# Optimization experiments

Measured on AMD Instinct MI355X. Metric: run time of the kernel, lower is better.

Reference implementation:

```python
import jax, jax.numpy as jnp
import numpy as np

DELTA = 1.0

def _lin(x, W, b):
    return x @ W + b

def _node(x, child_c, child_h, Wioux, bioux, Wiouh, biouh, Wfx, bfx, Wfh, bfh):
    # Child-sum TreeLSTM cell. x: [B, D]; child_c, child_h: [B, nc, M]
    h_sum = child_h.sum(axis=1)  # [B, M]
    iou = _lin(x, Wioux, bioux) + _lin(h_sum, Wiouh, biouh)  # [B, 3M]
    i, o, u = jnp.split(iou, 3, axis=-1)
    i, o, u = jax.nn.sigmoid(i), jax.nn.sigmoid(o), jnp.tanh(u)
    # forget gate per child: fh(child_h) + fx(x) broadcast over children
    f = jax.nn.sigmoid(_lin(child_h, Wfh, bfh) + _lin(x, Wfx, bfx)[:, None, :])  # [B, nc, M]
    c = i * u + (f * child_c).sum(axis=1)
    h = o * jnp.tanh(c)
    return c, h

def _treelstm(xs, Wioux, bioux, Wiouh, biouh, Wfx, bfx, Wfh, bfh):
    # xs: [B, 4, D]. Fixed 4-node tree: root = node 3, leaf children = {0,1,2}.
    # All leaves (same depth) are batched into one fused gate GEMM.
    B, _, D = xs.shape
    M = Wfx.shape[1]
    gates = (Wioux, bioux, Wiouh, biouh, Wfx, bfx, Wfh, bfh)
    x_leaf = xs[:, :3].reshape(B * 3, D)
    z = jnp.zeros((B * 3, 1, M), xs.dtype)  # leaves get zero child state
    c_l, h_l = _node(x_leaf, z, z, *gates)
    c_root, h_root = _node(xs[:, 3], c_l.reshape(B, 3, M), h_l.reshape(B, 3, M), *gates)
    return c_root, h_root

def setup_inputs() -> dict:
    key = jax.random.key(0)
    B, L, Lq, V, D, M, H, O = 512, 64, 128, 50000, 512, 512, 256, 30
    ks = jax.random.split(key, 24)
    ri = lambda k, shape: jax.random.randint(k, shape, 0, V)
    rn = lambda k, shape, s: jax.random.normal(k, shape, jnp.float32) * s
    return {
        'q_v': ri(ks[0], (B, L)), 'q_a0': ri(ks[1], (B, L)), 'n_a0': ri(ks[2], (B, L)),
        'q_a1': ri(ks[3], (B, L)), 'n_a1': ri(ks[4], (B, L)), 'q_a2': ri(ks[5], (B, L)),
        'n_a2': ri(ks[6], (B, L)),
        'query': ri(ks[7], (B, Lq)), 'pos': ri(ks[8], (B, Lq)), 'neg': ri(ks[9], (B, Lq)),
        'emb': rn(ks[10], (V, D), 0.02),
        'Wioux': rn(ks[11], (D, 3 * M), D ** -0.5), 'bioux': jnp.zeros((3 * M,), jnp.float32),
        'Wiouh': rn(ks[12], (M, 3 * M), M ** -0.5), 'biouh': jnp.zeros((3 * M,), jnp.float32),
        'Wfx': rn(ks[13], (D, M), D ** -0.5), 'bfx': jnp.zeros((M,), jnp.float32),
        'Wfh': rn(ks[14], (M, M), M ** -0.5), 'bfh': jnp.zeros((M,), jnp.float32),
        'Wwh': rn(ks[15], (M, H), M ** -0.5), 'bwh': jnp.zeros((H,), jnp.float32),
        'Wwp': rn(ks[16], (H, O), H ** -0.5), 'bwp': jnp.zeros((O,), jnp.float32),
    }

def reference(q_v, q_a0, n_a0, q_a1, n_a1, q_a2, n_a2, query, pos, neg,
              emb, Wioux, bioux, Wiouh, biouh, Wfx, bfx, Wfh, bfh, Wwh, bwh, Wwp, bwp):
    D = emb.shape[1]
    pool = lambda ids: emb[ids].mean(axis=1)  # embedding lookup + mean over tokens -> [B, D]
    qv = pool(q_v)
    def trip(qa, na):  # attribute-level triplet hinge loss, per batch row
        return jax.nn.relu(DELTA - (qv * pool(qa)).sum(-1) + (qv * pool(na)).sum(-1))
    loss = trip(q_a0, n_a0) + trip(q_a1, n_a1) + trip(q_a2, n_a2)
    def seq(ids):  # [B, Lq] -> 4 mean-pooled node vectors [B, 4, D]
        e = emb[ids]
        return e.reshape(e.shape[0], 4, -1, D).mean(axis=2)
    gates = (Wioux, bioux, Wiouh, biouh, Wfx, bfx, Wfh, bfh)
    qc, _ = _treelstm(seq(query), *gates)
    pc, _ = _treelstm(seq(pos), *gates)
    nc, _ = _treelstm(seq(neg), *gates)
    sim = lambda l, r: _lin(jax.nn.sigmoid(_lin(l * r, Wwh, bwh)), Wwp, bwp)  # Similarity module
    a = sim(qc, pc).sum(-1)
    b = sim(qc, nc).sum(-1)
    return loss + jax.nn.relu(DELTA - a + b)
```

## Files before the change

### kernel.cpp

```cpp
#include <hip/hip_runtime.h>
#include <hip/hip_bf16.h>


typedef __attribute__((ext_vector_type(8))) short short8;
typedef __attribute__((ext_vector_type(4))) float floatx4;
typedef __attribute__((ext_vector_type(2))) float floatx2;

__device__ inline ushort f2bf(float f) {
    unsigned u = __float_as_uint(f);
    u += 0x7fffu + ((u >> 16) & 1u);
    return (ushort)(u >> 16);
}
__device__ inline float bf2f(ushort u) { return __uint_as_float((unsigned)u << 16); }
__device__ inline float sigm(float x) { return 1.0f / (1.0f + expf(-x)); }

#if defined(__has_builtin)
#if __has_builtin(__builtin_amdgcn_cvt_pk_f32_fp8) && __has_builtin(__builtin_amdgcn_cvt_pk_fp8_f32)
#define HW_FP8 1
#endif
#endif

#ifndef HW_FP8
__device__ inline unsigned enc1(float x) {
    float a = fabsf(x);
    unsigned s = (__float_as_uint(x) >> 31) << 7;
    unsigned b = __float_as_uint(a);
    unsigned uexp = b >> 23;
    if (uexp < 121) {
        int m = (int)(a * 512.0f + 0.5f);
        if (m >= 8) return s | 0x08u;
        return s | (unsigned)m;
    }
    b += 0x00080000u;
    unsigned e = b >> 23;
    if (e > 135u) return s | 0x7Eu;
    return s | ((e - 120u) << 3) | ((b >> 20) & 7u);
}
__device__ inline float dec1(unsigned v) {
    unsigned s = (v >> 7) & 1u, e = (v >> 3) & 15u, m = v & 7u;
    float r = e ? __uint_as_float(((e + 120u) << 23) | (m << 20))
                : (float)m * 0.001953125f;
    return s ? -r : r;
}
#endif

__device__ inline unsigned pk4(float a, float b, float c, float d) {
#ifdef HW_FP8
    int v = 0;
    v = __builtin_amdgcn_cvt_pk_fp8_f32(a, b, v, false);
    v = __builtin_amdgcn_cvt_pk_fp8_f32(c, d, v, true);
    return (unsigned)v;
#else
    return enc1(a) | (enc1(b) << 8) | (enc1(c) << 16) | (enc1(d) << 24);
#endif
}
__device__ inline void dec4_add(unsigned v, float* acc) {
#ifdef HW_FP8
    floatx2 p0 = __builtin_amdgcn_cvt_pk_f32_fp8(v, false);
    floatx2 p1 = __builtin_amdgcn_cvt_pk_f32_fp8(v, true);
    acc[0] += p0[0]; acc[1] += p0[1]; acc[2] += p1[0]; acc[3] += p1[1];
#else
    acc[0] += dec1(v & 255u); acc[1] += dec1((v >> 8) & 255u);
    acc[2] += dec1((v >> 16) & 255u); acc[3] += dec1(v >> 24);
#endif
}

#define GLD16(gp, sp)                                                        \
    __builtin_amdgcn_global_load_lds(                                        \
        (const __attribute__((address_space(1))) unsigned int*)(const void*)(gp), \
        (__attribute__((address_space(3))) unsigned int*)(void*)(sp), 16, 0, 0)

#define FP8_SCALE 64.0f

__global__ __launch_bounds__(256) void prep_all_kernel(
    const float* __restrict__ emb, unsigned char* __restrict__ emb8,
    const float* __restrict__ Wioux, const float* __restrict__ Wiouh,
    const float* __restrict__ Wfh, const float* __restrict__ Wfx,
    const float* __restrict__ Wwh, const float* __restrict__ Wwp,
    const float* __restrict__ bwp,
    ushort* __restrict__ Wcat_t, ushort* __restrict__ Wfh_t,
    ushort* __restrict__ Wfx_t, ushort* __restrict__ Wwh_t,
    float* __restrict__ wsum) {
    __shared__ float tt[32][33];
    int blk = blockIdx.x, tid = threadIdx.x;
    if (blk < 12500) {
        size_t i = ((size_t)blk * 256 + tid) * 8;
        float4 a = *(const float4*)(emb + i);
        float4 b = *(const float4*)(emb + i + 4);
        uint2 o;
        o.x = pk4(a.x * FP8_SCALE, a.y * FP8_SCALE, a.z * FP8_SCALE, a.w * FP8_SCALE);
        o.y = pk4(b.x * FP8_SCALE, b.y * FP8_SCALE, b.z * FP8_SCALE, b.w * FP8_SCALE);
        *(uint2*)(emb8 + i) = o;
        return;
    }
    int tx = tid & 31, ty = tid >> 5;
    if (blk < 14036) {
        int idx = blk - 12500;
        int k0 = (idx & 31) * 32, n0 = (idx >> 5) * 32;
#pragma unroll
        for (int r = 0; r < 4; ++r) {
            int k = k0 + ty + r * 8;
            const float* s = (k < 512) ? Wioux + (size_t)k * 1536
                                       : Wiouh + (size_t)(k - 512) * 1536;
            tt[ty + r * 8][tx] = s[n0 + tx];
        }
        __syncthreads();
#pragma unroll
        for (int r = 0; r < 4; ++r)
            Wcat_t[(size_t)(n0 + ty + r * 8) * 1024 + k0 + tx] = f2bf(tt[tx][ty + r * 8]);
        return;
    }
    if (blk < 14676) {
        const float* W; ushort* Wt; int idx, ncols;
        if (blk < 14292)      { idx = blk - 14036; W = Wfh; Wt = Wfh_t; ncols = 512; }
        else if (blk < 14548) { idx = blk - 14292; W = Wfx; Wt = Wfx_t; ncols = 512; }
        else                  { idx = blk - 14548; W = Wwh; Wt = Wwh_t; ncols = 256; }
        int nt_count = ncols >> 5;
        int k0 = (idx / nt_count) * 32, n0 = (idx % nt_count) * 32;
#pragma unroll
        for (int r = 0; r < 4; ++r)
            tt[ty + r * 8][tx] = W[(size_t)(k0 + ty + r * 8) * ncols + n0 + tx];
        __syncthreads();
#pragma unroll
        for (int r = 0; r < 4; ++r)
            Wt[(size_t)(n0 + ty + r * 8) * 512 + k0 + tx] = f2bf(tt[tx][ty + r * 8]);
        return;
    }
    {
        float s = 0.f;
        for (int o = 0; o < 30; ++o) s += Wwp[tid * 30 + o];
        wsum[tid] = s;
        if (tid == 0) {
            float t = 0.f;
            for (int o = 0; o < 30; ++o) t += bwp[o];
            wsum[256] = t;
        }
    }
}

__global__ __launch_bounds__(256) void mega_gather_kernel(
    const int* __restrict__ q_v,
    const int* __restrict__ qa0, const int* __restrict__ na0,
    const int* __restrict__ qa1, const int* __restrict__ na1,
    const int* __restrict__ qa2, const int* __restrict__ na2,
    const int* __restrict__ query, const int* __restrict__ pos, const int* __restrict__ neg,
    const unsigned char* __restrict__ emb8,
    float* __restrict__ pools, ushort* __restrict__ Xleaf, ushort* __restrict__ XR) {
    __shared__ float sm[256][9];
    int tid = threadIdx.x;
    int c = tid & 63, g = tid >> 6;
    float acc[8] = {};
    if (blockIdx.x < 3584) {
        int s = blockIdx.x >> 9, b = blockIdx.x & 511;
        const int* aptr[7] = {q_v, qa0, na0, qa1, na1, qa2, na2};
        const int* ids = aptr[s] + b * 64 + g * 16;
#pragma unroll 8
        for (int t = 0; t < 16; ++t) {
            const uint2 v = *(const uint2*)(emb8 + (size_t)ids[t] * 512 + c * 8);
            dec4_add(v.x, acc);
            dec4_add(v.y, acc + 4);
        }
#pragma unroll
        for (int k = 0; k < 8; ++k) sm[tid][k] = acc[k];
        __syncthreads();
        if (tid < 64) {
#pragma unroll
            for (int gg = 1; gg < 4; ++gg)
#pragma unroll
                for (int k = 0; k < 8; ++k) acc[k] += sm[tid + gg * 64][k];
            const float sc = 1.0f / (64.0f * FP8_SCALE);
            float* dst = pools + ((size_t)s * 512 + b) * 512 + tid * 8;
            *(float4*)dst = make_float4(acc[0] * sc, acc[1] * sc, acc[2] * sc, acc[3] * sc);
            *(float4*)(dst + 4) = make_float4(acc[4] * sc, acc[5] * sc, acc[6] * sc, acc[7] * sc);
        }
    } else {
        int idx = blockIdx.x - 3584;
        int t = idx >> 11, rem = idx & 2047, b = rem >> 2, node = rem & 3;
        const int* sptr[3] = {query, pos, neg};
        const int* ids = sptr[t] + b * 128 + node * 32 + g * 8;
#pragma unroll
        for (int k = 0; k < 8; ++k) {
            const uint2 v = *(const uint2*)(emb8 + (size_t)ids[k] * 512 + c * 8);
            dec4_add(v.x, acc);
            dec4_add(v.y, acc + 4);
        }
#pragma unroll
        for (int k = 0; k < 8; ++k) sm[tid][k] = acc[k];
        __syncthreads();
        if (tid < 64) {
#pragma unroll
            for (int gg = 1; gg < 4; ++gg)
#pragma unroll
                for (int k = 0; k < 8; ++k) acc[k] += sm[tid + gg * 64][k];
            const float sc = 1.0f / (32.0f * FP8_SCALE);
            short8 o;
#pragma unroll
            for (int k = 0; k < 8; ++k) o[k] = (short)f2bf(acc[k] * sc);
            if (node < 3) {
                size_t r = ((size_t)(t * 512 + b)) * 3 + node;
                *(short8*)(Xleaf + r * 512 + tid * 8) = o;
            } else {
                size_t r = (size_t)(t * 512 + b);
                *(short8*)(XR + r * 1024 + tid * 8) = o;
            }
        }
    }
}

__global__ __launch_bounds__(256) void dots_kernel(const float* __restrict__ pools,
                                                   float* __restrict__ loss) {
    int b = blockIdx.x, tid = threadIdx.x;
    const float* pq = pools + (size_t)b * 512;
    float q0 = pq[tid], q1 = pq[tid + 256];
    float d[6];
#pragma unroll
    for (int a = 0; a < 6; ++a) {
        const float* pa = pools + ((size_t)(a + 1) * 512 + b) * 512;
        d[a] = q0 * pa[tid] + q1 * pa[tid + 256];
    }
    __shared__ float red[6][4];
    int lane = tid & 63, wid = tid >> 6;
#pragma unroll
    for (int a = 0; a < 6; ++a) {
        float v = d[a];
        for (int off = 32; off; off >>= 1) v += __shfl_down(v, off);
        if (lane == 0) red[a][wid] = v;
    }
    __syncthreads();
    if (tid == 0) {
        float l = 0.f;
#pragma unroll
        for (int i = 0; i < 3; ++i) {
            float dq = red[2*i][0] + red[2*i][1] + red[2*i][2] + red[2*i][3];
            float dn = red[2*i+1][0] + red[2*i+1][1] + red[2*i+1][2] + red[2*i+1][3];
            l += fmaxf(0.f, 1.f - dq + dn);
        }
        loss[b] = l;
    }
}

__device__ __forceinline__ void gemm_body(const ushort* __restrict__ A, int lda,
                                          const ushort* __restrict__ Bt, int ldb,
                                          float* __restrict__ C, int ldc, int K,
                                          int bx, int by, ushort* sA, ushort* sB) {
    int tid = threadIdx.x;
    int m0 = bx * 128, n0 = by * 128;
    int w = tid >> 6, lane = tid & 63;
    int wm = (w >> 1) * 64, wn = (w & 1) * 64;
    int l15 = lane & 15, g = lane >> 4;
    int srow = tid >> 2, scol = (tid & 3) * 8;

    const ushort* Ag0 = A + (size_t)(m0 + srow) * lda + scol;
    const ushort* Ag1 = A + (size_t)(m0 + srow + 64) * lda + scol;
    const ushort* Bg0 = Bt + (size_t)(n0 + srow) * ldb + scol;
    const ushort* Bg1 = Bt + (size_t)(n0 + srow + 64) * ldb + scol;
    ushort* sA0 = sA + w * 512;
    ushort* sA1 = sA + 2048 + w * 512;
    ushort* sB0 = sB + w * 512;
    ushort* sB1 = sB + 2048 + w * 512;

    floatx4 acc[4][4] = {};

    for (int kb = 0; kb < K; kb += 32) {
        __syncthreads();
        GLD16(Ag0 + kb, sA0);
        GLD16(Ag1 + kb, sA1);
        GLD16(Bg0 + kb, sB0);
        GLD16(Bg1 + kb, sB1);
        __syncthreads();
        short8 af[4], bf[4];
#pragma unroll
        for (int f = 0; f < 4; ++f) {
            af[f] = *(const short8*)(sA + (wm + f * 16 + l15) * 32 + g * 8);
            bf[f] = *(const short8*)(sB + (wn + f * 16 + l15) * 32 + g * 8);
        }
#pragma unroll
        for (int i = 0; i < 4; ++i)
#pragma unroll
            for (int j = 0; j < 4; ++j)
                acc[i][j] = __builtin_amdgcn_mfma_f32_16x16x32_bf16(af[i], bf[j], acc[i][j], 0, 0, 0);
    }
#pragma unroll
    for (int i = 0; i < 4; ++i)
#pragma unroll
        for (int j = 0; j < 4; ++j) {
            int row = m0 + wm + i * 16 + g * 4;
            int col = n0 + wn + j * 16 + l15;
#pragma unroll
            for (int r = 0; r < 4; ++r)
                C[(size_t)(row + r) * ldc + col] = acc[i][j][r];
        }
}

__global__ __launch_bounds__(256) void gemm_bf16(const ushort* __restrict__ A, int lda,
                                                 const ushort* __restrict__ Bt, int ldb,
                                                 float* __restrict__ C, int ldc, int K) {
    __shared__ alignas(16) ushort sA[128 * 32];
    __shared__ alignas(16) ushort sB[128 * 32];
    gemm_body(A, lda, Bt, ldb, C, ldc, K, blockIdx.x, blockIdx.y, sA, sB);
}

__global__ __launch_bounds__(256) void gemm3_bf16(
    const ushort* __restrict__ h_l, const ushort* __restrict__ XR,
    const ushort* __restrict__ Wfh_t, const ushort* __restrict__ Wfx_t,
    const ushort* __restrict__ Wcat_t,
    float* __restrict__ FH, float* __restrict__ FX, float* __restrict__ IOU_r) {
    __shared__ alignas(16) ushort sA[128 * 32];
    __shared__ alignas(16) ushort sB[128 * 32];
    int r = blockIdx.x;
    if (r < 144)      gemm_body(h_l, 512, Wfh_t, 512, FH, 512, 512, r % 36, r / 36, sA, sB);
    else if (r < 192) { int q = r - 144; gemm_body(XR, 1024, Wfx_t, 512, FX, 512, 512, q % 12, q / 12, sA, sB); }
    else              { int q = r - 192; gemm_body(XR, 1024, Wcat_t, 1024, IOU_r, 1536, 1024, q % 12, q / 12, sA, sB); }
}


__global__ __launch_bounds__(256) void leaf_act_kernel(
    const float* __restrict__ IOU_l, const float* __restrict__ bioux,
    const float* __restrict__ biouh, float* __restrict__ c_l,
    ushort* __restrict__ h_l, ushort* __restrict__ XR) {
    int tb = blockIdx.x, tid = threadIdx.x;
#pragma unroll
    for (int half = 0; half < 2; ++half) {
        int m = tid + half * 256;
        float bi = bioux[m] + biouh[m];
        float bo = bioux[m + 512] + biouh[m + 512];
        float bu = bioux[m + 1024] + biouh[m + 1024];
        float hs = 0.f;
#pragma unroll
        for (int leaf = 0; leaf < 3; ++leaf) {
            size_t r = (size_t)tb * 3 + leaf;
            const float* row = IOU_l + r * 1536;
            float iv = sigm(row[m] + bi);
            float ov = sigm(row[m + 512] + bo);
            float uv = tanhf(row[m + 1024] + bu);
            float c = iv * uv;
            c_l[r * 512 + m] = c;
            float h = ov * tanhf(c);
            h_l[r * 512 + m] = f2bf(h);
            hs += h;
        }
        XR[(size_t)tb * 1024 + 512 + m] = f2bf(hs);
    }
}

__global__ __launch_bounds__(256) void root_act_kernel(
    const float* __restrict__ IOU_r, const float* __restrict__ FH,
    const float* __restrict__ FX, const float* __restrict__ c_l,
    const float* __restrict__ bioux, const float* __restrict__ biouh,
    const float* __restrict__ bfx, const float* __restrict__ bfh,
    float* __restrict__ c_root) {
    int r = blockIdx.x, tid = threadIdx.x;
#pragma unroll
    for (int half = 0; half < 2; ++half) {
        int m = tid + half * 256;
        float iv = sigm(IOU_r[(size_t)r * 1536 + m] + bioux[m] + biouh[m]);
        float uv = tanhf(IOU_r[(size_t)r * 1536 + 1024 + m] + bioux[1024 + m] + biouh[1024 + m]);
        float fx = FX[(size_t)r * 512 + m] + bfx[m];
        float c = iv * uv;
#pragma unroll
        for (int k = 0; k < 3; ++k) {
            size_t idx = ((size_t)r * 3 + k) * 512 + m;
            float f = sigm(FH[idx] + bfh[m] + fx);
            c += f * c_l[idx];
        }
        c_root[(size_t)r * 512 + m] = c;
    }
}

__global__ __launch_bounds__(256) void prod_kernel(const float* __restrict__ c_root,
                                                   ushort* __restrict__ P) {
    int e = blockIdx.x * 256 + threadIdx.x;
    int row = e >> 9, n = e & 511;
    int b = row & 511, which = row >> 9;
    float q = c_root[(size_t)b * 512 + n];
    float o = c_root[((size_t)(which + 1) * 512 + b) * 512 + n];
    P[e] = f2bf(q * o);
}

__global__ __launch_bounds__(256) void final_kernel(
    const float* __restrict__ S, const float* __restrict__ bwh,
    const float* __restrict__ wsum, const float* __restrict__ loss,
    float* __restrict__ out) {
    int b = blockIdx.x, tid = threadIdx.x;
    float w = wsum[tid];
    float bw = bwh[tid];
    float va = sigm(S[(size_t)b * 256 + tid] + bw) * w;
    float vb = sigm(S[(size_t)(512 + b) * 256 + tid] + bw) * w;
    int lane = tid & 63, wid = tid >> 6;
    for (int off = 32; off; off >>= 1) {
        va += __shfl_down(va, off);
        vb += __shfl_down(vb, off);
    }
    __shared__ float ra[4], rb[4];
    if (lane == 0) { ra[wid] = va; rb[wid] = vb; }
    __syncthreads();
    if (tid == 0) {
        float a  = ra[0] + ra[1] + ra[2] + ra[3] + wsum[256];
        float bb = rb[0] + rb[1] + rb[2] + rb[3] + wsum[256];
        out[b] = loss[b] + fmaxf(0.f, 1.f - a + bb);
    }
}


extern "C" void kernel_launch(void* const* d_in, const int* in_sizes, int n_in,
                              void* d_out, int out_size, void* d_ws, size_t ws_size,
                              hipStream_t stream) {
    const int* q_v   = (const int*)d_in[0];
    const int* q_a0  = (const int*)d_in[1];
    const int* n_a0  = (const int*)d_in[2];
    const int* q_a1  = (const int*)d_in[3];
    const int* n_a1  = (const int*)d_in[4];
    const int* q_a2  = (const int*)d_in[5];
    const int* n_a2  = (const int*)d_in[6];
    const int* query = (const int*)d_in[7];
    const int* pos   = (const int*)d_in[8];
    const int* neg   = (const int*)d_in[9];
    const float* emb   = (const float*)d_in[10];
    const float* Wioux = (const float*)d_in[11];
    const float* bioux = (const float*)d_in[12];
    const float* Wiouh = (const float*)d_in[13];
    const float* biouh = (const float*)d_in[14];
    const float* Wfx   = (const float*)d_in[15];
    const float* bfx   = (const float*)d_in[16];
    const float* Wfh   = (const float*)d_in[17];
    const float* bfh   = (const float*)d_in[18];
    const float* Wwh   = (const float*)d_in[19];
    const float* bwh   = (const float*)d_in[20];
    const float* Wwp   = (const float*)d_in[21];
    const float* bwp   = (const float*)d_in[22];
    float* out = (float*)d_out;

    char* w = (char*)d_ws;
    size_t off = 0;
    auto alloc = [&](size_t bytes) -> void* {
        void* p = (void*)(w + off);
        off = (off + bytes + 255) & ~(size_t)255;
        return p;
    };
    ushort* Wcat_t = (ushort*)alloc((size_t)1536 * 1024 * 2);
    ushort* Wfh_t  = (ushort*)alloc((size_t)512 * 512 * 2);
    ushort* Wfx_t  = (ushort*)alloc((size_t)512 * 512 * 2);
    ushort* Wwh_t  = (ushort*)alloc((size_t)256 * 512 * 2);
    float*  wsum   = (float*) alloc(257 * 4);
    float*  lossv  = (float*) alloc(512 * 4);
    ushort* Xleaf  = (ushort*)alloc((size_t)4608 * 512 * 2);
    ushort* XR     = (ushort*)alloc((size_t)1536 * 1024 * 2);
    size_t xbase = off;
    unsigned char* emb8 = (unsigned char*)alloc((size_t)50000 * 512);
    float* pools        = (float*)        alloc((size_t)7 * 512 * 512 * 4);
    off = xbase;
    float*  IOU_l  = (float*) alloc((size_t)4608 * 1536 * 4);
    float*  c_l    = (float*) alloc((size_t)4608 * 512 * 4);
    ushort* h_l    = (ushort*)alloc((size_t)4608 * 512 * 2);
    float*  FH     = (float*) alloc((size_t)4608 * 512 * 4);
    float*  FX     = (float*) alloc((size_t)1536 * 512 * 4);
    float*  IOU_r  = (float*) alloc((size_t)1536 * 1536 * 4);
    float*  c_root = (float*) alloc((size_t)1536 * 512 * 4);
    ushort* P      = (ushort*)alloc((size_t)1024 * 512 * 2);
    float*  S      = (float*) alloc((size_t)1024 * 256 * 4);

    prep_all_kernel<<<14677, 256, 0, stream>>>(emb, emb8, Wioux, Wiouh, Wfh, Wfx, Wwh,
                                               Wwp, bwp, Wcat_t, Wfh_t, Wfx_t, Wwh_t, wsum);
    mega_gather_kernel<<<9728, 256, 0, stream>>>(q_v, q_a0, n_a0, q_a1, n_a1, q_a2, n_a2,
                                                 query, pos, neg, emb8, pools, Xleaf, XR);
    dots_kernel<<<512, 256, 0, stream>>>(pools, lossv);

    gemm_bf16<<<dim3(36, 12), 256, 0, stream>>>(Xleaf, 512, Wcat_t, 1024, IOU_l, 1536, 512);
    leaf_act_kernel<<<1536, 256, 0, stream>>>(IOU_l, bioux, biouh, c_l, h_l, XR);
    gemm3_bf16<<<336, 256, 0, stream>>>(h_l, XR, Wfh_t, Wfx_t, Wcat_t, FH, FX, IOU_r);
    root_act_kernel<<<1536, 256, 0, stream>>>(IOU_r, FH, FX, c_l, bioux, biouh, bfx, bfh, c_root);

    prod_kernel<<<2048, 256, 0, stream>>>(c_root, P);
    gemm_bf16<<<dim3(8, 2), 256, 0, stream>>>(P, 512, Wwh_t, 512, S, 256, 512);
    final_kernel<<<512, 256, 0, stream>>>(S, bwh, wsum, lossv, out);
}
```

Measured before the change: 134.3 us.

## Double-buffer GEMMs, store intermediates in bf16, fuse dots and prod into GEMMs

Gather loops now issue all embedding loads before decoding, to get more memory-level parallelism. The GEMM body double-buffers its LDS tiles so the next K-slice loads while MFMAs run on the current one. The dots reduction is merged into the leaf GEMM launch, and the elementwise product is computed inside the similarity GEMM's A staging, which removes two launches. IOU, FH, FX and c_l intermediates are stored as bf16 to halve their traffic, at some cost in precision.

```diff
diff --git a/kernel.cpp b/kernel.cpp
--- a/kernel.cpp
+++ b/kernel.cpp
@@ -154,12 +154,12 @@
         int s = blockIdx.x >> 9, b = blockIdx.x & 511;
         const int* aptr[7] = {q_v, qa0, na0, qa1, na1, qa2, na2};
         const int* ids = aptr[s] + b * 64 + g * 16;
-#pragma unroll 8
-        for (int t = 0; t < 16; ++t) {
-            const uint2 v = *(const uint2*)(emb8 + (size_t)ids[t] * 512 + c * 8);
-            dec4_add(v.x, acc);
-            dec4_add(v.y, acc + 4);
-        }
+        uint2 v[16];
+#pragma unroll
+        for (int t = 0; t < 16; ++t)
+            v[t] = *(const uint2*)(emb8 + (size_t)ids[t] * 512 + c * 8);
+#pragma unroll
+        for (int t = 0; t < 16; ++t) { dec4_add(v[t].x, acc); dec4_add(v[t].y, acc + 4); }
 #pragma unroll
         for (int k = 0; k < 8; ++k) sm[tid][k] = acc[k];
         __syncthreads();
@@ -178,12 +178,12 @@
         int t = idx >> 11, rem = idx & 2047, b = rem >> 2, node = rem & 3;
         const int* sptr[3] = {query, pos, neg};
         const int* ids = sptr[t] + b * 128 + node * 32 + g * 8;
-#pragma unroll
-        for (int k = 0; k < 8; ++k) {
-            const uint2 v = *(const uint2*)(emb8 + (size_t)ids[k] * 512 + c * 8);
-            dec4_add(v.x, acc);
-            dec4_add(v.y, acc + 4);
-        }
+        uint2 v[8];
+#pragma unroll
+        for (int k = 0; k < 8; ++k)
+            v[k] = *(const uint2*)(emb8 + (size_t)ids[k] * 512 + c * 8);
+#pragma unroll
+        for (int k = 0; k < 8; ++k) { dec4_add(v[k].x, acc); dec4_add(v[k].y, acc + 4); }
 #pragma unroll
         for (int k = 0; k < 8; ++k) sm[tid][k] = acc[k];
         __syncthreads();
@@ -207,41 +207,13 @@
     }
 }
 
-__global__ __launch_bounds__(256) void dots_kernel(const float* __restrict__ pools,
-                                                   float* __restrict__ loss) {
-    int b = blockIdx.x, tid = threadIdx.x;
-    const float* pq = pools + (size_t)b * 512;
-    float q0 = pq[tid], q1 = pq[tid + 256];
-    float d[6];
-#pragma unroll
-    for (int a = 0; a < 6; ++a) {
-        const float* pa = pools + ((size_t)(a + 1) * 512 + b) * 512;
-        d[a] = q0 * pa[tid] + q1 * pa[tid + 256];
-    }
-    __shared__ float red[6][4];
-    int lane = tid & 63, wid = tid >> 6;
-#pragma unroll
-    for (int a = 0; a < 6; ++a) {
-        float v = d[a];
-        for (int off = 32; off; off >>= 1) v += __shfl_down(v, off);
-        if (lane == 0) red[a][wid] = v;
-    }
-    __syncthreads();
-    if (tid == 0) {
-        float l = 0.f;
-#pragma unroll
-        for (int i = 0; i < 3; ++i) {
-            float dq = red[2*i][0] + red[2*i][1] + red[2*i][2] + red[2*i][3];
-            float dn = red[2*i+1][0] + red[2*i+1][1] + red[2*i+1][2] + red[2*i+1][3];
-            l += fmaxf(0.f, 1.f - dq + dn);
-        }
-        loss[b] = l;
-    }
-}
-
+__device__ inline void cstore(float* C, size_t idx, float v)  { C[idx] = v; }
+__device__ inline void cstore(ushort* C, size_t idx, float v) { C[idx] = f2bf(v); }
+
+template <typename OutT>
 __device__ __forceinline__ void gemm_body(const ushort* __restrict__ A, int lda,
                                           const ushort* __restrict__ Bt, int ldb,
-                                          float* __restrict__ C, int ldc, int K,
+                                          OutT* __restrict__ C, int ldc, int K,
                                           int bx, int by, ushort* sA, ushort* sB) {
     int tid = threadIdx.x;
     int m0 = bx * 128, n0 = by * 128;
@@ -254,31 +226,38 @@
     const ushort* Ag1 = A + (size_t)(m0 + srow + 64) * lda + scol;
     const ushort* Bg0 = Bt + (size_t)(n0 + srow) * ldb + scol;
     const ushort* Bg1 = Bt + (size_t)(n0 + srow + 64) * ldb + scol;
-    ushort* sA0 = sA + w * 512;
-    ushort* sA1 = sA + 2048 + w * 512;
-    ushort* sB0 = sB + w * 512;
-    ushort* sB1 = sB + 2048 + w * 512;
 
     floatx4 acc[4][4] = {};
 
+    auto stage = [&](int buf, int kb) {
+        ushort* dA = sA + buf * 4096;
+        ushort* dB = sB + buf * 4096;
+        GLD16(Ag0 + kb, dA + w * 512);
+        GLD16(Ag1 + kb, dA + 2048 + w * 512);
+        GLD16(Bg0 + kb, dB + w * 512);
+        GLD16(Bg1 + kb, dB + 2048 + w * 512);
+    };
+
+    stage(0, 0);
+    __syncthreads();
+    int cur = 0;
     for (int kb = 0; kb < K; kb += 32) {
-        __syncthreads();
-        GLD16(Ag0 + kb, sA0);
-        GLD16(Ag1 + kb, sA1);
-        GLD16(Bg0 + kb, sB0);
-        GLD16(Bg1 + kb, sB1);
-        __syncthreads();
+        if (kb + 32 < K) stage(cur ^ 1, kb + 32);
+        const ushort* bA = sA + cur * 4096;
+        const ushort* bB = sB + cur * 4096;
         short8 af[4], bf[4];
 #pragma unroll
         for (int f = 0; f < 4; ++f) {
-            af[f] = *(const short8*)(sA + (wm + f * 16 + l15) * 32 + g * 8);
-            bf[f] = *(const short8*)(sB + (wn + f * 16 + l15) * 32 + g * 8);
+            af[f] = *(const short8*)(bA + (wm + f * 16 + l15) * 32 + g * 8);
+            bf[f] = *(const short8*)(bB + (wn + f * 16 + l15) * 32 + g * 8);
         }
 #pragma unroll
         for (int i = 0; i < 4; ++i)
 #pragma unroll
             for (int j = 0; j < 4; ++j)
                 acc[i][j] = __builtin_amdgcn_mfma_f32_16x16x32_bf16(af[i], bf[j], acc[i][j], 0, 0, 0);
+        __syncthreads();
+        cur ^= 1;
     }
 #pragma unroll
     for (int i = 0; i < 4; ++i)
@@ -288,35 +267,141 @@
             int col = n0 + wn + j * 16 + l15;
 #pragma unroll
             for (int r = 0; r < 4; ++r)
-                C[(size_t)(row + r) * ldc + col] = acc[i][j][r];
-        }
-}
-
-__global__ __launch_bounds__(256) void gemm_bf16(const ushort* __restrict__ A, int lda,
-                                                 const ushort* __restrict__ Bt, int ldb,
-                                                 float* __restrict__ C, int ldc, int K) {
-    __shared__ alignas(16) ushort sA[128 * 32];
-    __shared__ alignas(16) ushort sB[128 * 32];
-    gemm_body(A, lda, Bt, ldb, C, ldc, K, blockIdx.x, blockIdx.y, sA, sB);
-}
-
-__global__ __launch_bounds__(256) void gemm3_bf16(
+                cstore(C, (size_t)(row + r) * ldc + col, acc[i][j][r]);
+        }
+}
+
+__global__ __launch_bounds__(256) void g1_dots_kernel(
+    const ushort* __restrict__ Xleaf, const ushort* __restrict__ Wcat_t,
+    ushort* __restrict__ IOU_l,
+    const float* __restrict__ pools, float* __restrict__ lossv) {
+    __shared__ alignas(16) ushort sA[8192];
+    __shared__ alignas(16) ushort sB[8192];
+    __shared__ float red[6][4];
+    int blk = blockIdx.x, tid = threadIdx.x;
+    if (blk < 432) {
+        gemm_body(Xleaf, 512, Wcat_t, 1024, IOU_l, 1536, 512, blk % 36, blk / 36, sA, sB);
+        return;
+    }
+    int b = blk - 432;
+    const float* pq = pools + (size_t)b * 512;
+    float q0 = pq[tid], q1 = pq[tid + 256];
+    float d[6];
+#pragma unroll
+    for (int a = 0; a < 6; ++a) {
+        const float* pa = pools + ((size_t)(a + 1) * 512 + b) * 512;
+        d[a] = q0 * pa[tid] + q1 * pa[tid + 256];
+    }
+    int lane = tid & 63, wid = tid >> 6;
+#pragma unroll
+    for (int a = 0; a < 6; ++a) {
+        float v = d[a];
+        for (int off = 32; off; off >>= 1) v += __shfl_down(v, off);
+        if (lane == 0) red[a][wid] = v;
+    }
+    __syncthreads();
+    if (tid == 0) {
+        float l = 0.f;
+#pragma unroll
+        for (int i = 0; i < 3; ++i) {
+            float dq = red[2*i][0] + red[2*i][1] + red[2*i][2] + red[2*i][3];
+            float dn = red[2*i+1][0] + red[2*i+1][1] + red[2*i+1][2] + red[2*i+1][3];
+            l += fmaxf(0.f, 1.f - dq + dn);
+        }
+        lossv[b] = l;
+    }
+}
+
+__global__ __launch_bounds__(256) void gemm3_kernel(
     const ushort* __restrict__ h_l, const ushort* __restrict__ XR,
     const ushort* __restrict__ Wfh_t, const ushort* __restrict__ Wfx_t,
     const ushort* __restrict__ Wcat_t,
-    float* __restrict__ FH, float* __restrict__ FX, float* __restrict__ IOU_r) {
-    __shared__ alignas(16) ushort sA[128 * 32];
-    __shared__ alignas(16) ushort sB[128 * 32];
+    ushort* __restrict__ FH, ushort* __restrict__ FX, ushort* __restrict__ IOU_r) {
+    __shared__ alignas(16) ushort sA[8192];
+    __shared__ alignas(16) ushort sB[8192];
     int r = blockIdx.x;
-    if (r < 144)      gemm_body(h_l, 512, Wfh_t, 512, FH, 512, 512, r % 36, r / 36, sA, sB);
-    else if (r < 192) { int q = r - 144; gemm_body(XR, 1024, Wfx_t, 512, FX, 512, 512, q % 12, q / 12, sA, sB); }
-    else              { int q = r - 192; gemm_body(XR, 1024, Wcat_t, 1024, IOU_r, 1536, 1024, q % 12, q / 12, sA, sB); }
+    if (r < 144)      gemm_body(XR, 1024, Wcat_t, 1024, IOU_r, 1536, 1024, r % 12, r / 12, sA, sB);
+    else if (r < 288) { int q = r - 144; gemm_body(h_l, 512, Wfh_t, 512, FH, 512, 512, q % 36, q / 36, sA, sB); }
+    else              { int q = r - 288; gemm_body(XR, 1024, Wfx_t, 512, FX, 512, 512, q % 12, q / 12, sA, sB); }
+}
+
+__global__ __launch_bounds__(256) void gemm_sim_kernel(
+    const float* __restrict__ c_root, const ushort* __restrict__ Wwh_t,
+    float* __restrict__ S) {
+    __shared__ alignas(16) ushort sA[8192];
+    __shared__ alignas(16) ushort sB[8192];
+    int tid = threadIdx.x;
+    int bx = blockIdx.x & 7, by = blockIdx.x >> 3;
+    int m0 = bx * 128, n0 = by * 128;
+    int w = tid >> 6, lane = tid & 63;
+    int wm = (w >> 1) * 64, wn = (w & 1) * 64;
+    int l15 = lane & 15, g = lane >> 4;
+    int srow = tid >> 2, scol = (tid & 3) * 8;
+
+    const ushort* Bg0 = Wwh_t + (size_t)(n0 + srow) * 512 + scol;
+    const ushort* Bg1 = Wwh_t + (size_t)(n0 + srow + 64) * 512 + scol;
+
+    floatx4 acc[4][4] = {};
+
+    auto stage = [&](int buf, int kb) {
+        ushort* dA = sA + buf * 4096;
+        ushort* dB = sB + buf * 4096;
+        GLD16(Bg0 + kb, dB + w * 512);
+        GLD16(Bg1 + kb, dB + 2048 + w * 512);
+#pragma unroll
+        for (int half = 0; half < 2; ++half) {
+            int gr = m0 + srow + half * 64;
+            int b = gr & 511, which = gr >> 9;
+            const float* qrow = c_root + (size_t)b * 512 + kb + scol;
+            const float* orow = c_root + ((size_t)(which + 1) * 512 + b) * 512 + kb + scol;
+            float4 q0 = *(const float4*)qrow, q1 = *(const float4*)(qrow + 4);
+            float4 o0 = *(const float4*)orow, o1 = *(const float4*)(orow + 4);
+            short8 pv;
+            pv[0] = (short)f2bf(q0.x * o0.x); pv[1] = (short)f2bf(q0.y * o0.y);
+            pv[2] = (short)f2bf(q0.z * o0.z); pv[3] = (short)f2bf(q0.w * o0.w);
+            pv[4] = (short)f2bf(q1.x * o1.x); pv[5] = (short)f2bf(q1.y * o1.y);
+            pv[6] = (short)f2bf(q1.z * o1.z); pv[7] = (short)f2bf(q1.w * o1.w);
+            *(short8*)(dA + (srow + half * 64) * 32 + scol) = pv;
+        }
+    };
+
+    stage(0, 0);
+    __syncthreads();
+    int cur = 0;
+    for (int kb = 0; kb < 512; kb += 32) {
+        if (kb + 32 < 512) stage(cur ^ 1, kb + 32);
+        const ushort* bA = sA + cur * 4096;
+        const ushort* bB = sB + cur * 4096;
+        short8 af[4], bf[4];
+#pragma unroll
+        for (int f = 0; f < 4; ++f) {
+            af[f] = *(const short8*)(bA + (wm + f * 16 + l15) * 32 + g * 8);
+            bf[f] = *(const short8*)(bB + (wn + f * 16 + l15) * 32 + g * 8);
+        }
+#pragma unroll
+        for (int i = 0; i < 4; ++i)
+#pragma unroll
+            for (int j = 0; j < 4; ++j)
+                acc[i][j] = __builtin_amdgcn_mfma_f32_16x16x32_bf16(af[i], bf[j], acc[i][j], 0, 0, 0);
+        __syncthreads();
+        cur ^= 1;
+    }
+#pragma unroll
+    for (int i = 0; i < 4; ++i)
+#pragma unroll
+        for (int j = 0; j < 4; ++j) {
+            int row = m0 + wm + i * 16 + g * 4;
+            int col = n0 + wn + j * 16 + l15;
+#pragma unroll
+            for (int r = 0; r < 4; ++r)
+                S[(size_t)(row + r) * 256 + col] = acc[i][j][r];
+        }
 }
 
 
 __global__ __launch_bounds__(256) void leaf_act_kernel(
-    const float* __restrict__ IOU_l, const float* __restrict__ bioux,
-    const float* __restrict__ biouh, float* __restrict__ c_l,
+    const ushort* __restrict__ IOU_l, const float* __restrict__ bioux,
+    const float* __restrict__ biouh, ushort* __restrict__ c_l,
     ushort* __restrict__ h_l, ushort* __restrict__ XR) {
     int tb = blockIdx.x, tid = threadIdx.x;
 #pragma unroll
@@ -329,12 +414,12 @@
 #pragma unroll
         for (int leaf = 0; leaf < 3; ++leaf) {
             size_t r = (size_t)tb * 3 + leaf;
-            const float* row = IOU_l + r * 1536;
-            float iv = sigm(row[m] + bi);
-            float ov = sigm(row[m + 512] + bo);
-            float uv = tanhf(row[m + 1024] + bu);
+            const ushort* row = IOU_l + r * 1536;
+            float iv = sigm(bf2f(row[m]) + bi);
+            float ov = sigm(bf2f(row[m + 512]) + bo);
+            float uv = tanhf(bf2f(row[m + 1024]) + bu);
             float c = iv * uv;
-            c_l[r * 512 + m] = c;
+            c_l[r * 512 + m] = f2bf(c);
             float h = ov * tanhf(c);
             h_l[r * 512 + m] = f2bf(h);
             hs += h;
@@ -344,8 +429,8 @@
 }
 
 __global__ __launch_bounds__(256) void root_act_kernel(
-    const float* __restrict__ IOU_r, const float* __restrict__ FH,
-    const float* __restrict__ FX, const float* __restrict__ c_l,
+    const ushort* __restrict__ IOU_r, const ushort* __restrict__ FH,
+    const ushort* __restrict__ FX, const ushort* __restrict__ c_l,
     const float* __restrict__ bioux, const float* __restrict__ biouh,
     const float* __restrict__ bfx, const float* __restrict__ bfh,
     float* __restrict__ c_root) {
@@ -353,28 +438,18 @@
 #pragma unroll
     for (int half = 0; half < 2; ++half) {
         int m = tid + half * 256;
-        float iv = sigm(IOU_r[(size_t)r * 1536 + m] + bioux[m] + biouh[m]);
-        float uv = tanhf(IOU_r[(size_t)r * 1536 + 1024 + m] + bioux[1024 + m] + biouh[1024 + m]);
-        float fx = FX[(size_t)r * 512 + m] + bfx[m];
+        float iv = sigm(bf2f(IOU_r[(size_t)r * 1536 + m]) + bioux[m] + biouh[m]);
+        float uv = tanhf(bf2f(IOU_r[(size_t)r * 1536 + 1024 + m]) + bioux[1024 + m] + biouh[1024 + m]);
+        float fx = bf2f(FX[(size_t)r * 512 + m]) + bfx[m];
         float c = iv * uv;
 #pragma unroll
         for (int k = 0; k < 3; ++k) {
             size_t idx = ((size_t)r * 3 + k) * 512 + m;
-            float f = sigm(FH[idx] + bfh[m] + fx);
-            c += f * c_l[idx];
+            float f = sigm(bf2f(FH[idx]) + bfh[m] + fx);
+            c += f * bf2f(c_l[idx]);
         }
         c_root[(size_t)r * 512 + m] = c;
     }
-}
-
-__global__ __launch_bounds__(256) void prod_kernel(const float* __restrict__ c_root,
-                                                   ushort* __restrict__ P) {
-    int e = blockIdx.x * 256 + threadIdx.x;
-    int row = e >> 9, n = e & 511;
-    int b = row & 511, which = row >> 9;
-    float q = c_root[(size_t)b * 512 + n];
-    float o = c_root[((size_t)(which + 1) * 512 + b) * 512 + n];
-    P[e] = f2bf(q * o);
 }
 
 __global__ __launch_bounds__(256) void final_kernel(
@@ -449,28 +524,23 @@
     unsigned char* emb8 = (unsigned char*)alloc((size_t)50000 * 512);
     float* pools        = (float*)        alloc((size_t)7 * 512 * 512 * 4);
     off = xbase;
-    float*  IOU_l  = (float*) alloc((size_t)4608 * 1536 * 4);
-    float*  c_l    = (float*) alloc((size_t)4608 * 512 * 4);
+    ushort* IOU_l  = (ushort*)alloc((size_t)4608 * 1536 * 2);
+    ushort* c_l    = (ushort*)alloc((size_t)4608 * 512 * 2);
     ushort* h_l    = (ushort*)alloc((size_t)4608 * 512 * 2);
-    float*  FH     = (float*) alloc((size_t)4608 * 512 * 4);
-    float*  FX     = (float*) alloc((size_t)1536 * 512 * 4);
-    float*  IOU_r  = (float*) alloc((size_t)1536 * 1536 * 4);
+    ushort* FH     = (ushort*)alloc((size_t)4608 * 512 * 2);
+    ushort* FX     = (ushort*)alloc((size_t)1536 * 512 * 2);
+    ushort* IOU_r  = (ushort*)alloc((size_t)1536 * 1536 * 2);
     float*  c_root = (float*) alloc((size_t)1536 * 512 * 4);
-    ushort* P      = (ushort*)alloc((size_t)1024 * 512 * 2);
     float*  S      = (float*) alloc((size_t)1024 * 256 * 4);
 
     prep_all_kernel<<<14677, 256, 0, stream>>>(emb, emb8, Wioux, Wiouh, Wfh, Wfx, Wwh,
                                                Wwp, bwp, Wcat_t, Wfh_t, Wfx_t, Wwh_t, wsum);
     mega_gather_kernel<<<9728, 256, 0, stream>>>(q_v, q_a0, n_a0, q_a1, n_a1, q_a2, n_a2,
                                                  query, pos, neg, emb8, pools, Xleaf, XR);
-    dots_kernel<<<512, 256, 0, stream>>>(pools, lossv);
-
-    gemm_bf16<<<dim3(36, 12), 256, 0, stream>>>(Xleaf, 512, Wcat_t, 1024, IOU_l, 1536, 512);
+    g1_dots_kernel<<<944, 256, 0, stream>>>(Xleaf, Wcat_t, IOU_l, pools, lossv);
     leaf_act_kernel<<<1536, 256, 0, stream>>>(IOU_l, bioux, biouh, c_l, h_l, XR);
-    gemm3_bf16<<<336, 256, 0, stream>>>(h_l, XR, Wfh_t, Wfx_t, Wcat_t, FH, FX, IOU_r);
+    gemm3_kernel<<<336, 256, 0, stream>>>(h_l, XR, Wfh_t, Wfx_t, Wcat_t, FH, FX, IOU_r);
     root_act_kernel<<<1536, 256, 0, stream>>>(IOU_r, FH, FX, c_l, bioux, biouh, bfx, bfh, c_root);
-
-    prod_kernel<<<2048, 256, 0, stream>>>(c_root, P);
-    gemm_bf16<<<dim3(8, 2), 256, 0, stream>>>(P, 512, Wwh_t, 512, S, 256, 512);
+    gemm_sim_kernel<<<16, 256, 0, stream>>>(c_root, Wwh_t, S);
     final_kernel<<<512, 256, 0, stream>>>(S, bwh, wsum, lossv, out);
 }
```

After: 124.5 us. -7.3%, faster.
